# Optimization experiments

Measured on AMD Instinct MI355X. Metric: run time of the kernel, lower is better.

Reference implementation:

```python
import jax, jax.numpy as jnp
import numpy as np

NUM_HEADS = 12

def setup_inputs() -> dict:
    key = jax.random.key(0)
    ks = jax.random.split(key, 8)
    B, N, C = 8, 1024, 768
    H = NUM_HEADS
    return {
        "x": jax.random.normal(ks[0], (B, N, C), dtype=jnp.float32),
        "relative_position_index": jax.random.randint(ks[1], (N, N), 0, 2048, dtype=jnp.int64),
        "qkv_weight": jax.random.normal(ks[2], (3 * C, C), dtype=jnp.float32) * 0.02,
        "q_bias": jax.random.normal(ks[3], (C,), dtype=jnp.float32) * 0.02,
        "v_bias": jax.random.normal(ks[4], (C,), dtype=jnp.float32) * 0.02,
        "proj_weight": jax.random.normal(ks[5], (C, C), dtype=jnp.float32) * 0.02,
        "proj_bias": jax.random.normal(ks[6], (C,), dtype=jnp.float32) * 0.02,
        "rel_pos_bias_table": jax.random.normal(ks[7], (2048, H), dtype=jnp.float32) * 0.02,
    }

def reference(x, relative_position_index, qkv_weight, q_bias, v_bias, proj_weight, proj_bias, rel_pos_bias_table):
    B, N, C = x.shape
    H = NUM_HEADS
    d = C // H
    scale = d ** (-0.5)
    # qkv bias: (q_bias, zeros, v_bias) as in the torch module
    qkv_b = jnp.concatenate([q_bias, jnp.zeros_like(v_bias), v_bias])
    qkv = x @ qkv_weight.T + qkv_b  # [B,N,3C]
    qkv = qkv.reshape(B, N, 3, H, d).transpose(2, 0, 3, 1, 4)  # [3,B,H,N,d]
    q, k, v = qkv[0], qkv[1], qkv[2]
    attn = jnp.einsum("bhnd,bhmd->bhnm", q * scale, k)  # [B,H,N,N]
    # relative position bias: table lookup [N,N,H] -> [H,N,N]
    bias = rel_pos_bias_table[relative_position_index].transpose(2, 0, 1)
    attn = attn + bias[None]
    attn = jax.nn.softmax(attn, axis=-1)
    out = jnp.einsum("bhnm,bhmd->bhnd", attn, v)  # [B,H,N,d]
    out = out.transpose(0, 2, 1, 3).reshape(B, N, C)
    return out @ proj_weight.T + proj_bias
```

## Files before the change

kernel.cpp:

```cpp
#include <hip/hip_runtime.h>

typedef unsigned short ushort_t;
typedef __bf16 bf16x8 __attribute__((ext_vector_type(8)));
typedef float f32x4 __attribute__((ext_vector_type(4)));
typedef unsigned int u32x4 __attribute__((ext_vector_type(4)));

#define MFMA(a, b, c) __builtin_amdgcn_mfma_f32_16x16x32_bf16((a), (b), (c), 0, 0, 0)

#define BATCH 8
#define SEQ 1024
#define CDIM 768
#define NH 12
#define HD 64
#define MTOT (BATCH * SEQ)
#define THREEC (3 * CDIM)
#define KVB 64
#define LOG2E 1.44269504088896f

__device__ __forceinline__ ushort_t f2bf(float f) {
    unsigned int u = __builtin_bit_cast(unsigned int, f);
    u = (u + 0x7FFFu + ((u >> 16) & 1u)) >> 16;
    return (ushort_t)u;
}
__device__ __forceinline__ float bf2f(ushort_t b) {
    unsigned int u = ((unsigned int)b) << 16;
    return __builtin_bit_cast(float, u);
}
__device__ __forceinline__ ushort_t bfbits(float f) {
    __bf16 h = (__bf16)f;
    return __builtin_bit_cast(ushort_t, h);
}
__device__ __forceinline__ unsigned int pack2bf(float a, float b) {
    ushort2 p;
    p.x = bfbits(a);
    p.y = bfbits(b);
    return __builtin_bit_cast(unsigned int, p);
}

typedef const __attribute__((address_space(1))) unsigned int* gas_ptr;
typedef __attribute__((address_space(3))) unsigned int* las_ptr;

__device__ __forceinline__ void async16(const ushort_t* g, ushort_t* l) {
    __builtin_amdgcn_global_load_lds((gas_ptr)(const void*)g, (las_ptr)(void*)l, 16, 0, 0);
}

#define WAITVM_(N) asm volatile("s_waitcnt vmcnt(" #N ")" ::: "memory")
#define WAITVM(N) WAITVM_(N)
#define SCHEDB __builtin_amdgcn_sched_barrier(0)

__global__ __launch_bounds__(256) void k_convert(const float* __restrict__ x,
                                                 const float* __restrict__ wq,
                                                 const float* __restrict__ wp,
                                                 ushort_t* __restrict__ xb,
                                                 ushort_t* __restrict__ wqb,
                                                 ushort_t* __restrict__ wpb) {
    const int NX = MTOT * CDIM / 4;
    const int NQ = THREEC * CDIM / 4;
    const int NP = CDIM * CDIM / 4;
    int i = blockIdx.x * 256 + threadIdx.x;
    const float4* src;
    ushort_t* dst;
    int off;
    if (i < NX) { src = (const float4*)x; dst = xb; off = i; }
    else if (i < NX + NQ) { src = (const float4*)wq; dst = wqb; off = i - NX; }
    else if (i < NX + NQ + NP) { src = (const float4*)wp; dst = wpb; off = i - NX - NQ; }
    else return;
    float4 v = src[off];
    ushort4 o;
    o.x = f2bf(v.x); o.y = f2bf(v.y); o.z = f2bf(v.z); o.w = f2bf(v.w);
    ((ushort4*)dst)[off] = o;
}

__global__ __launch_bounds__(256) void k_bias(const int* __restrict__ rpi,
                                              const float* __restrict__ table,
                                              ushort_t* __restrict__ biasF) {
    __shared__ int idx_s[16][64];
    int tr = blockIdx.x;
    int tcq = blockIdx.y;
    int t = threadIdx.x;
    {
        int r = t >> 4;
        int c4 = (t & 15) * 4;
        int4 v = *(const int4*)&rpi[(tr * 16 + r) * SEQ + tcq * 64 + c4];
        *(int4*)&idx_s[r][c4] = v;
    }
    __syncthreads();
    int j = t >> 6;
    int lane = t & 63;
    int lq = lane >> 4, l15 = lane & 15;
    int tc = tcq * 4 + j;
    int id[4];
#pragma unroll
    for (int rr = 0; rr < 4; rr++) id[rr] = idx_s[l15][j * 16 + lq * 4 + rr];
#pragma unroll
    for (int h = 0; h < NH; h++) {
        ushort4 o;
        o.x = f2bf(table[id[0] * NH + h] * LOG2E);
        o.y = f2bf(table[id[1] * NH + h] * LOG2E);
        o.z = f2bf(table[id[2] * NH + h] * LOG2E);
        o.w = f2bf(table[id[3] * NH + h] * LOG2E);
        *(ushort4*)&biasF[(((h * 64 + tr) * 64 + tc) * 256 + lane * 4)] = o;
    }
}

template <int MODE>
__global__ __launch_bounds__(256) void k_gemm(const ushort_t* __restrict__ A,
                                              const ushort_t* __restrict__ Bw,
                                              const float* __restrict__ biasq,
                                              const float* __restrict__ biasv,
                                              const float* __restrict__ biasp,
                                              ushort_t* __restrict__ qb,
                                              ushort_t* __restrict__ kb,
                                              ushort_t* __restrict__ vT,
                                              float* __restrict__ outp) {
    __shared__ __attribute__((aligned(16))) ushort_t As[128 * 64];
    __shared__ __attribute__((aligned(16))) ushort_t Bs[128 * 64];
    const int K = CDIM;
    int tid = threadIdx.x, wave = tid >> 6, lane = tid & 63;
    int l15 = lane & 15, lq = lane >> 4;
    int wm = wave >> 1, wn = wave & 1;
    int nx = gridDim.x;
    int bidl = blockIdx.y * nx + blockIdx.x;
    int chunk = (nx * gridDim.y) >> 3;
    int swz = (bidl & 7) * chunk + (bidl >> 3);
    int colBase = (swz % nx) * 128;
    int rowBase = (swz / nx) * 128;
    f32x4 acc[4][4] = {};
    int srow = wave * 8 + (lane >> 3);
    int scol = (((lane & 7) ^ (srow & 7))) * 8;
    int l7 = l15 & 7;
    for (int k0 = 0; k0 < K; k0 += 64) {
#pragma unroll
        for (int is = 0; is < 4; is++) {
            async16(A + (rowBase + is * 32 + srow) * K + k0 + scol,
                    As + is * 2048 + tid * 8);
            async16(Bw + (colBase + is * 32 + srow) * K + k0 + scol,
                    Bs + is * 2048 + tid * 8);
        }
        asm volatile("s_waitcnt vmcnt(0)" ::: "memory");
        __syncthreads();
#pragma unroll
        for (int kk = 0; kk < 64; kk += 32) {
            bf16x8 af[4], bfr[4];
#pragma unroll
            for (int mf = 0; mf < 4; mf++)
                af[mf] = *(const bf16x8*)&As[(wm * 64 + mf * 16 + l15) * 64 +
                                             ((((kk >> 3) + lq) ^ l7) * 8)];
#pragma unroll
            for (int nf = 0; nf < 4; nf++)
                bfr[nf] = *(const bf16x8*)&Bs[(wn * 64 + nf * 16 + l15) * 64 +
                                              ((((kk >> 3) + lq) ^ l7) * 8)];
#pragma unroll
            for (int mf = 0; mf < 4; mf++)
#pragma unroll
                for (int nf = 0; nf < 4; nf++)
                    acc[mf][nf] = MFMA(af[mf], bfr[nf], acc[mf][nf]);
        }
        __syncthreads();
    }
#pragma unroll
    for (int mf = 0; mf < 4; mf++) {
#pragma unroll
        for (int nf = 0; nf < 4; nf++) {
            int jc = colBase + wn * 64 + nf * 16 + l15;
            int mg0 = rowBase + wm * 64 + mf * 16 + (lane >> 4) * 4;
            if (MODE == 0) {
                int which = jc / CDIM;
                int co = jc - which * CDIM;
                int b = mg0 >> 10, tok0 = mg0 & 1023;
                int hh = co >> 6, dd = co & 63;
                int bh = b * NH + hh;
                if (which == 0) {
                    float bq_ = biasq[co];
#pragma unroll
                    for (int r = 0; r < 4; r++)
                        qb[(bh * SEQ + tok0 + r) * HD + dd] =
                            f2bf((acc[mf][nf][r] + bq_) * 0.125f);
                } else if (which == 1) {
#pragma unroll
                    for (int r = 0; r < 4; r++)
                        kb[(bh * SEQ + tok0 + r) * HD + dd] = f2bf(acc[mf][nf][r]);
                } else {
                    float bv = biasv[co];
                    ushort4 pk;
                    pk.x = f2bf(acc[mf][nf][0] + bv);
                    pk.y = f2bf(acc[mf][nf][1] + bv);
                    pk.z = f2bf(acc[mf][nf][2] + bv);
                    pk.w = f2bf(acc[mf][nf][3] + bv);
                    *(ushort4*)&vT[(size_t)(bh * HD + dd) * SEQ + tok0] = pk;
                }
            } else {
                float bp_ = biasp[jc];
#pragma unroll
                for (int r = 0; r < 4; r++)
                    outp[(size_t)(mg0 + r) * CDIM + jc] = acc[mf][nf][r] + bp_;
            }
        }
    }
}

__global__ __launch_bounds__(256, 4) void k_attn(const ushort_t* __restrict__ qb,
                                                 const ushort_t* __restrict__ kb,
                                                 const ushort_t* __restrict__ vT,
                                                 const ushort_t* __restrict__ biasF,
                                                 ushort_t* __restrict__ ctx) {
    __shared__ __attribute__((aligned(16))) ushort_t Ks[2][KVB * 64];
    __shared__ __attribute__((aligned(16))) ushort_t Vs[2][KVB * 64];

    int lin = ((int)blockIdx.x & 7) * 192 + ((int)blockIdx.x >> 3);
    int h = lin >> 7;
    int b = (lin >> 4) & 7;
    int qt = lin & 15;
    int bh = b * NH + h;
    int tid = threadIdx.x, w = tid >> 6, lane = tid & 63;
    int l15 = lane & 15, lq = lane >> 4, lq4 = lq * 4;
    int row0 = qt * 64 + w * 16;
    int qtile0 = row0 >> 4;

    const ushort_t* qp = qb + bh * SEQ * HD;
    const ushort_t* kp = kb + bh * SEQ * HD;
    const ushort_t* vp = vT + bh * HD * SEQ;
    const ushort_t* bfp = biasF + (size_t)(h * 64 + qtile0) * 64 * 256;

    int lamA = l15 + 32 * (lq & 1);
    int lamB = lamA + 16;

    int rk0, sk0, rk1, sk1;
    {
        int cid0 = tid;
        rk0 = cid0 >> 3; sk0 = ((cid0 & 7) ^ (rk0 & 7)) * 8;
        int cid1 = 256 + tid;
        rk1 = cid1 >> 3; sk1 = ((cid1 & 7) ^ (rk1 & 7)) * 8;
    }

#define STAGE_K(BUF, C0)                                                    \
    do {                                                                    \
        async16(kp + ((C0) + rk0) * HD + sk0, &Ks[BUF][tid * 8]);           \
        async16(kp + ((C0) + rk1) * HD + sk1, &Ks[BUF][(256 + tid) * 8]);   \
    } while (0)
#define STAGE_V(BUF, C0)                                                    \
    do {                                                                    \
        async16(vp + rk0 * SEQ + (C0) + sk0, &Vs[BUF][tid * 8]);            \
        async16(vp + rk1 * SEQ + (C0) + sk1, &Vs[BUF][(256 + tid) * 8]);    \
    } while (0)
#define LOAD_BIAS(DST, T)                                                   \
    do {                                                                    \
        int kt0 = (T) * 4;                                                  \
        _Pragma("unroll") for (int n = 0; n < 4; n++)                       \
            (DST)[n] = *(const ushort4*)&bfp[(kt0 + n) * 256 + lane * 4];   \
    } while (0)

    bf16x8 qfr0 = *(const bf16x8*)&qp[(row0 + l15) * HD + 8 * lq];
    bf16x8 qfr1 = *(const bf16x8*)&qp[(row0 + l15) * HD + 32 + 8 * lq];

    f32x4 Oa[4] = {};
    float li = 0.0f;
    f32x4 accA[4], accB[4];
    ushort4 bfrP[4], bfrQ[4];
    unsigned int u0[4][2];

#define QK_BLOCK(AN, KN)                                                       \
    do {                                                                       \
        __builtin_amdgcn_s_setprio(1);                                         \
        _Pragma("unroll") for (int n = 0; n < 4; n++) {                        \
            int krow = n * 16 + l15;                                           \
            bf16x8 kf0 = *(const bf16x8*)&(KN)[krow * 64 + ((lq ^ (krow & 7)) * 8)]; \
            bf16x8 kf1 = *(const bf16x8*)&(KN)[krow * 64 + (((lq + 4) ^ (krow & 7)) * 8)]; \
            f32x4 z0 = {};                                                     \
            z0 = MFMA(kf0, qfr0, z0); z0 = MFMA(kf1, qfr1, z0);                \
            (AN)[n] = z0;                                                      \
        }                                                                      \
        __builtin_amdgcn_s_setprio(0);                                         \
    } while (0)

#define SOFTMAX_STEP(ACC, BFR)                                                 \
    do {                                                                       \
        f32x4 sv = {};                                                         \
        _Pragma("unroll") for (int n = 0; n < 4; n++) {                        \
            float p0 = exp2f(fmaf((ACC)[n][0], LOG2E, bf2f((BFR)[n].x)));      \
            float p1 = exp2f(fmaf((ACC)[n][1], LOG2E, bf2f((BFR)[n].y)));      \
            float p2 = exp2f(fmaf((ACC)[n][2], LOG2E, bf2f((BFR)[n].z)));      \
            float p3 = exp2f(fmaf((ACC)[n][3], LOG2E, bf2f((BFR)[n].w)));      \
            sv[0] += p0; sv[1] += p1; sv[2] += p2; sv[3] += p3;                \
            u0[n][0] = pack2bf(p0, p1);                                        \
            u0[n][1] = pack2bf(p2, p3);                                        \
        }                                                                      \
        li += (sv[0] + sv[1]) + (sv[2] + sv[3]);                               \
    } while (0)

#define ASSEMBLE(KS, PF)                                                       \
    do {                                                                       \
        unsigned int a0 = __shfl((int)u0[2 * (KS)][0], lamA);                  \
        unsigned int b0 = __shfl((int)u0[2 * (KS) + 1][0], lamA);              \
        unsigned int a1 = __shfl((int)u0[2 * (KS)][1], lamA);                  \
        unsigned int b1 = __shfl((int)u0[2 * (KS) + 1][1], lamA);              \
        unsigned int a2 = __shfl((int)u0[2 * (KS)][0], lamB);                  \
        unsigned int b2 = __shfl((int)u0[2 * (KS) + 1][0], lamB);              \
        unsigned int a3 = __shfl((int)u0[2 * (KS)][1], lamB);                  \
        unsigned int b3 = __shfl((int)u0[2 * (KS) + 1][1], lamB);              \
        bool hi_ = (lq & 2) != 0;                                              \
        u32x4 qd;                                                              \
        qd[0] = hi_ ? b0 : a0; qd[1] = hi_ ? b1 : a1;                          \
        qd[2] = hi_ ? b2 : a2; qd[3] = hi_ ? b3 : a3;                          \
        (PF) = __builtin_bit_cast(bf16x8, qd);                                 \
    } while (0)

#define PV_BLOCK(VC)                                                           \
    do {                                                                       \
        __builtin_amdgcn_s_setprio(1);                                         \
        _Pragma("unroll") for (int ks = 0; ks < 2; ks++) {                     \
            bf16x8 pfa;                                                        \
            ASSEMBLE(ks, pfa);                                                 \
            _Pragma("unroll") for (int nc = 0; nc < 4; nc++) {                 \
                int vrow = nc * 16 + l15;                                      \
                bf16x8 vf = *(const bf16x8*)&(VC)[vrow * 64 + (((ks * 4 + lq) ^ (vrow & 7)) * 8)]; \
                Oa[nc] = MFMA(pfa, vf, Oa[nc]);                                \
            }                                                                  \
        }                                                                      \
        __builtin_amdgcn_s_setprio(0);                                         \
    } while (0)

#define ITER(T, AC, AN, BC, BN, DO_KST, DO_VST, DO_QK)                         \
    do {                                                                       \
        WAITVM(0);                                                             \
        SCHEDB;                                                                \
        __builtin_amdgcn_s_barrier();                                          \
        SCHEDB;                                                                \
        const int t_ = (T);                                                    \
        if (DO_KST) STAGE_K(t_ & 1, (t_ + 2) * KVB);                           \
        if (DO_VST) STAGE_V((t_ + 1) & 1, (t_ + 1) * KVB);                     \
        if (DO_QK) LOAD_BIAS(BN, t_ + 1);                                      \
        if (DO_QK) QK_BLOCK(AN, Ks[(t_ + 1) & 1]);                             \
        SOFTMAX_STEP(AC, BC);                                                  \
        PV_BLOCK(Vs[t_ & 1]);                                                  \
    } while (0)

    STAGE_K(0, 0);
    STAGE_V(0, 0);
    STAGE_K(1, KVB);
    LOAD_BIAS(bfrP, 0);
    WAITVM(0);
    SCHEDB;
    __builtin_amdgcn_s_barrier();
    SCHEDB;
    QK_BLOCK(accA, Ks[0]);

#pragma unroll 1
    for (int tt = 0; tt < 14; tt += 2) {
        ITER(tt,     accA, accB, bfrP, bfrQ, 1, 1, 1);
        ITER(tt + 1, accB, accA, bfrQ, bfrP, 1, 1, 1);
    }
    ITER(14, accA, accB, bfrP, bfrQ, 0, 1, 1);
    ITER(15, accB, accA, bfrQ, bfrP, 0, 0, 0);

    float lsum = li;
    lsum += __shfl_xor(lsum, 16);
    lsum += __shfl_xor(lsum, 32);
    float rli = 1.0f / lsum;
#pragma unroll
    for (int r = 0; r < 4; r++) {
        float rl = __shfl(rli, (lane & 48) | (lq4 + r));
#pragma unroll
        for (int nc = 0; nc < 4; nc++) {
            ctx[(size_t)(b * SEQ + row0 + lq4 + r) * CDIM + h * HD + nc * 16 + l15] =
                bfbits(Oa[nc][r] * rl);
        }
    }
#undef ITER
#undef PV_BLOCK
#undef ASSEMBLE
#undef SOFTMAX_STEP
#undef QK_BLOCK
#undef LOAD_BIAS
#undef STAGE_V
#undef STAGE_K
}

extern "C" void kernel_launch(void* const* d_in, const int* in_sizes, int n_in,
                              void* d_out, int out_size, void* d_ws, size_t ws_size,
                              hipStream_t stream) {
    const float* x = (const float*)d_in[0];
    const int* rpi = (const int*)d_in[1];
    const float* wqkv = (const float*)d_in[2];
    const float* qbias = (const float*)d_in[3];
    const float* vbias = (const float*)d_in[4];
    const float* wproj = (const float*)d_in[5];
    const float* pbias = (const float*)d_in[6];
    const float* table = (const float*)d_in[7];
    float* out = (float*)d_out;

    char* ws = (char*)d_ws;
    ushort_t* xb    = (ushort_t*)(ws + 0);
    ushort_t* wqb   = (ushort_t*)(ws + 12582912);
    ushort_t* wpb   = (ushort_t*)(ws + 16121856);
    ushort_t* qbuf  = (ushort_t*)(ws + 17301504);
    ushort_t* kbuf  = (ushort_t*)(ws + 29884416);
    ushort_t* vTbuf = (ushort_t*)(ws + 42467328);
    ushort_t* ctx   = (ushort_t*)(ws + 55050240);
    ushort_t* biasF = (ushort_t*)(ws + 67633152);

    k_convert<<<8448, 256, 0, stream>>>(x, wqkv, wproj, xb, wqb, wpb);
    k_bias<<<dim3(64, 16), 256, 0, stream>>>(rpi, table, biasF);
    k_gemm<0><<<dim3(THREEC / 128, MTOT / 128), 256, 0, stream>>>(
        xb, wqb, qbias, vbias, nullptr, qbuf, kbuf, vTbuf, nullptr);
    k_attn<<<1536, 256, 0, stream>>>(qbuf, kbuf, vTbuf, biasF, ctx);
    k_gemm<1><<<dim3(CDIM / 128, MTOT / 128), 256, 0, stream>>>(
        ctx, wpb, nullptr, nullptr, pbias, nullptr, nullptr, nullptr, out);
}
```

Measured before the change: 160.9 us.

## Double-buffer GEMM LDS tiles with 32-wide K steps to overlap loads

The projection GEMM kernel now splits K into 32-wide steps with two LDS buffers. It issues the async global-to-LDS copy for the next step before running the MFMAs on the current one, where the old code loaded a 64-wide tile and waited before computing. The swizzle changes to fit 32-element rows. This hides global load latency behind compute, at the cost of twice as many barriers and waits per K.

```diff
diff --git a/kernel.cpp b/kernel.cpp
--- a/kernel.cpp
+++ b/kernel.cpp
@@ -113,9 +113,10 @@
                                               ushort_t* __restrict__ kb,
                                               ushort_t* __restrict__ vT,
                                               float* __restrict__ outp) {
-    __shared__ __attribute__((aligned(16))) ushort_t As[128 * 64];
-    __shared__ __attribute__((aligned(16))) ushort_t Bs[128 * 64];
+    __shared__ __attribute__((aligned(16))) ushort_t As[2][128 * 32];
+    __shared__ __attribute__((aligned(16))) ushort_t Bs[2][128 * 32];
     const int K = CDIM;
+    const int NSTEP = K / 32;
     int tid = threadIdx.x, wave = tid >> 6, lane = tid & 63;
     int l15 = lane & 15, lq = lane >> 4;
     int wm = wave >> 1, wn = wave & 1;
@@ -126,36 +127,44 @@
     int colBase = (swz % nx) * 128;
     int rowBase = (swz / nx) * 128;
     f32x4 acc[4][4] = {};
-    int srow = wave * 8 + (lane >> 3);
-    int scol = (((lane & 7) ^ (srow & 7))) * 8;
-    int l7 = l15 & 7;
-    for (int k0 = 0; k0 < K; k0 += 64) {
-#pragma unroll
-        for (int is = 0; is < 4; is++) {
-            async16(A + (rowBase + is * 32 + srow) * K + k0 + scol,
-                    As + is * 2048 + tid * 8);
-            async16(Bw + (colBase + is * 32 + srow) * K + k0 + scol,
-                    Bs + is * 2048 + tid * 8);
-        }
-        asm volatile("s_waitcnt vmcnt(0)" ::: "memory");
-        __syncthreads();
-#pragma unroll
-        for (int kk = 0; kk < 64; kk += 32) {
-            bf16x8 af[4], bfr[4];
-#pragma unroll
-            for (int mf = 0; mf < 4; mf++)
-                af[mf] = *(const bf16x8*)&As[(wm * 64 + mf * 16 + l15) * 64 +
-                                             ((((kk >> 3) + lq) ^ l7) * 8)];
+    int rr = tid >> 2;
+    int pp = ((tid & 3) ^ (rr & 3)) * 8;
+    int l3 = l15 & 3;
+
+#define GSTAGE(BUF, K0)                                                        \
+    do {                                                                       \
+        async16(A + (rowBase + rr) * K + (K0) + pp, &As[BUF][tid * 8]);        \
+        async16(A + (rowBase + 64 + rr) * K + (K0) + pp,                       \
+                &As[BUF][(256 + tid) * 8]);                                    \
+        async16(Bw + (colBase + rr) * K + (K0) + pp, &Bs[BUF][tid * 8]);       \
+        async16(Bw + (colBase + 64 + rr) * K + (K0) + pp,                      \
+                &Bs[BUF][(256 + tid) * 8]);                                    \
+    } while (0)
+
+    GSTAGE(0, 0);
+    WAITVM(0);
+    __syncthreads();
+#pragma unroll 1
+    for (int kt = 0; kt < NSTEP; kt++) {
+        if (kt + 1 < NSTEP) GSTAGE((kt + 1) & 1, (kt + 1) * 32);
+        const ushort_t* Ab = &As[kt & 1][0];
+        const ushort_t* Bb = &Bs[kt & 1][0];
+        bf16x8 af[4], bfr[4];
+#pragma unroll
+        for (int mf = 0; mf < 4; mf++)
+            af[mf] = *(const bf16x8*)&Ab[(wm * 64 + mf * 16 + l15) * 32 +
+                                         ((lq ^ l3) * 8)];
+#pragma unroll
+        for (int nf = 0; nf < 4; nf++)
+            bfr[nf] = *(const bf16x8*)&Bb[(wn * 64 + nf * 16 + l15) * 32 +
+                                          ((lq ^ l3) * 8)];
+#pragma unroll
+        for (int mf = 0; mf < 4; mf++)
 #pragma unroll
             for (int nf = 0; nf < 4; nf++)
-                bfr[nf] = *(const bf16x8*)&Bs[(wn * 64 + nf * 16 + l15) * 64 +
-                                              ((((kk >> 3) + lq) ^ l7) * 8)];
-#pragma unroll
-            for (int mf = 0; mf < 4; mf++)
-#pragma unroll
-                for (int nf = 0; nf < 4; nf++)
-                    acc[mf][nf] = MFMA(af[mf], bfr[nf], acc[mf][nf]);
-        }
+                acc[mf][nf] = MFMA(af[mf], bfr[nf], acc[mf][nf]);
+        WAITVM(0);
+        SCHEDB;
         __syncthreads();
     }
 #pragma unroll
@@ -197,6 +206,7 @@
             }
         }
     }
+#undef GSTAGE
 }
 
 __global__ __launch_bounds__(256, 4) void k_attn(const ushort_t* __restrict__ qb,
```

New measurement: 166.9 us. 1.04x slower.
